# Kernel tuning notes

Measured on AMD Instinct MI355X. Metric: run time of the kernel, lower is better.

The kernel has to match this reference:

```python
import jax, jax.numpy as jnp
import numpy as np

N_NODES = 50000
N_EDGES = 600000
N_RELS = 19
D_IN = 128
D_HID = 64
D_OUT = 2


def setup_inputs() -> dict:
    key = jax.random.key(0)
    ks = jax.random.split(key, 10)
    feat = jax.random.normal(ks[0], (N_NODES, D_IN), dtype=jnp.float32)
    src = jax.random.randint(ks[1], (N_EDGES,), 0, N_NODES)
    dst = jax.random.randint(ks[2], (N_EDGES,), 0, N_NODES)
    etype = jax.random.randint(ks[3], (N_EDGES,), 0, N_RELS)
    s1 = 1.0 / np.sqrt(D_IN)
    s2 = 1.0 / np.sqrt(D_HID)
    W1 = jax.random.normal(ks[4], (N_RELS, D_IN, D_HID), dtype=jnp.float32) * s1
    loop1 = jax.random.normal(ks[5], (D_IN, D_HID), dtype=jnp.float32) * s1
    b1 = jnp.zeros((D_HID,), dtype=jnp.float32)
    W2 = jax.random.normal(ks[6], (N_RELS, D_HID, D_OUT), dtype=jnp.float32) * s2
    loop2 = jax.random.normal(ks[7], (D_HID, D_OUT), dtype=jnp.float32) * s2
    b2 = jnp.zeros((D_OUT,), dtype=jnp.float32)
    return {"feat": feat, "W1": W1, "loop1": loop1, "b1": b1,
            "W2": W2, "loop2": loop2, "b2": b2,
            "src": src, "dst": dst, "etype": etype}


def _rel_graph_conv(h, W, loop_w, bias, src, dst, etype, activation):
    # Per-relation transform of all nodes: [N, R, O]; then gather per edge.
    # (num_rels * out_feat is small, so this is cheaper than gathering W per edge.)
    transformed = jnp.einsum('nd,rdo->nro', h, W)
    msg = transformed[src, etype]                      # [E, O] edge messages
    agg = jax.ops.segment_sum(msg, dst, num_segments=h.shape[0])  # scatter-add
    out = agg + h @ loop_w + bias                      # self-loop + bias
    if activation is not None:
        out = activation(out)
    return out


def reference(feat, W1, loop1, b1, W2, loop2, b2, src, dst, etype):
    h = _rel_graph_conv(feat, W1, loop1, b1, src, dst, etype, jax.nn.relu)
    h = _rel_graph_conv(h, W2, loop2, b2, src, dst, etype, None)
    return h
```

## Files before the change

kernel.cpp:

```cpp
#include <hip/hip_runtime.h>

#define N_NODES 50000
#define N_EDGES 600000
#define N_RELS  19
#define D_IN    128
#define D_HID   64
#define D_OUT   2
#define EDGE_TILES ((N_EDGES + 127) / 128 + N_RELS)
#define SL_BLOCKS  ((N_NODES + 63) / 64)

typedef unsigned short u16;
typedef unsigned int   u32;
typedef __attribute__((ext_vector_type(8))) short sfrag;
typedef __attribute__((ext_vector_type(4))) float f32x4;

__device__ __forceinline__ u16 f2bf(float f){
  union { float f; u32 i; } v; v.f = f;
  u32 r = v.i + 0x7fffu + ((v.i >> 16) & 1u);
  return (u16)(r >> 16);
}
__device__ __forceinline__ float bf2f(u16 u){
  union { u32 i; float f; } v; v.i = ((u32)u) << 16; return v.f;
}

__global__ void k_prep(const float* __restrict__ W1, const float* __restrict__ loop1,
                       const float* __restrict__ W2,
                       u16* __restrict__ W1Tb, u16* __restrict__ loop1Tb,
                       u16* __restrict__ W2Tb, int* __restrict__ hist_rel,
                       int* __restrict__ hist_dst, int* __restrict__ gcnt){
  int idx = blockIdx.x * 256 + threadIdx.x;
  if (idx < N_RELS)  hist_rel[idx] = 0;
  if (idx < N_NODES) hist_dst[idx] = 0;
  if (idx == 0) gcnt[0] = 0;
  const int T1 = N_RELS * D_HID * D_IN;
  const int T2 = T1 + N_RELS * 16 * D_HID;
  const int T3 = T2 + D_HID * D_IN;
  if (idx < T1) {
    int r = idx / (D_HID * D_IN);
    int t = idx - r * (D_HID * D_IN);
    int j = t >> 7, d = t & 127;
    W1Tb[idx] = f2bf(W1[(r * D_IN + d) * D_HID + j]);
  } else if (idx < T2) {
    int k2 = idx - T1;
    int r = k2 / (16 * D_HID);
    int t = k2 - r * (16 * D_HID);
    int n = t >> 6, k = t & 63;
    W2Tb[k2] = (n < D_OUT) ? f2bf(W2[(r * D_HID + k) * D_OUT + n]) : (u16)0;
  } else if (idx < T3) {
    int k2 = idx - T2;
    int j = k2 >> 7, d = k2 & 127;
    loop1Tb[k2] = f2bf(loop1[d * D_HID + j]);
  }
}

__global__ __launch_bounds__(256) void k_fused_pre(const float* __restrict__ feat,
                                                   u16* __restrict__ featb,
                                                   const int* __restrict__ et,
                                                   const int* __restrict__ dst,
                                                   int* __restrict__ hist_rel,
                                                   int* __restrict__ hist_dst){
  int i = blockIdx.x * 256 + threadIdx.x;
  float2 f = ((const float2*)feat)[i];
  ((u32*)featb)[i] = (u32)f2bf(f.x) | ((u32)f2bf(f.y) << 16);
  if (blockIdx.x < (N_EDGES + 255) / 256) {
    __shared__ int lh[N_RELS];
    int tid = threadIdx.x;
    if (tid < N_RELS) lh[tid] = 0;
    __syncthreads();
    int e = blockIdx.x * 256 + tid;
    if (e < N_EDGES) {
      atomicAdd(&lh[et[e]], 1);
      atomicAdd(&hist_dst[dst[e]], 1);
    }
    __syncthreads();
    if (tid < N_RELS && lh[tid]) atomicAdd(&hist_rel[tid], lh[tid]);
  }
}

__global__ __launch_bounds__(256) void k_alloc_scan(
    const int* __restrict__ hist_dst, int* __restrict__ dstart,
    int* __restrict__ cur_dst, int* __restrict__ gcnt,
    const int* __restrict__ hist_rel, int* __restrict__ offs,
    int* __restrict__ toff, int* __restrict__ cur_rel){
  if (blockIdx.x == 196) {
    if (threadIdx.x == 0) {
      int acc = 0, tacc = 0;
      offs[0] = 0; toff[0] = 0;
      for (int r = 0; r < N_RELS; ++r) {
        cur_rel[r] = acc;
        int c = hist_rel[r];
        acc += c;                offs[r + 1] = acc;
        tacc += (c + 127) >> 7;  toff[r + 1] = tacc;
      }
    }
    return;
  }
  __shared__ int wbase[4];
  int tid = threadIdx.x, lane = tid & 63, wv = tid >> 6;
  int n = blockIdx.x * 256 + tid;
  int v = (n < N_NODES) ? hist_dst[n] : 0;
  int x = v;
  #pragma unroll
  for (int o = 1; o < 64; o <<= 1) { int u = __shfl_up(x, o); if (lane >= o) x += u; }
  if (lane == 63) wbase[wv] = atomicAdd(gcnt, x);
  __syncthreads();
  int start = wbase[wv] + x - v;
  if (n < N_NODES) { dstart[n] = start; cur_dst[n] = start; }
}

__global__ __launch_bounds__(256) void k_scatter_rel(const int* __restrict__ et,
                                                     int* __restrict__ cursor,
                                                     int* __restrict__ perm){
  __shared__ int lh[N_RELS], base[N_RELS];
  int tid = threadIdx.x;
  if (tid < N_RELS) lh[tid] = 0;
  __syncthreads();
  int e = blockIdx.x * 256 + tid;
  int r = 0, my = 0;
  bool valid = e < N_EDGES;
  if (valid) { r = et[e]; my = atomicAdd(&lh[r], 1); }
  __syncthreads();
  if (tid < N_RELS && lh[tid]) base[tid] = atomicAdd(&cursor[tid], lh[tid]);
  __syncthreads();
  if (valid) perm[base[r] + my] = e;
}

__global__ __launch_bounds__(256) void k_se1(
    const u16* __restrict__ featb, const u16* __restrict__ W1Tb,
    const u16* __restrict__ loop1Tb, const float* __restrict__ b1,
    const int* __restrict__ src, const int* __restrict__ dst,
    const int* __restrict__ perm, const int* __restrict__ offs,
    const int* __restrict__ toff, int* __restrict__ cur_dst,
    u16* __restrict__ msgbuf, float* __restrict__ agg1f){
  __shared__ __align__(16) u16 Als[128][136];
  __shared__ int posIds[128];
  int tid = threadIdx.x, lane = tid & 63, w = tid >> 6;
  int r16 = lane & 15, c4 = lane >> 4;

  if (blockIdx.x >= EDGE_TILES) {
    int base = (blockIdx.x - EDGE_TILES) * 64;
    { int i = tid >> 2, seg = tid & 3;
      int n = base + i; if (n >= N_NODES) n = N_NODES - 1;
      const uint4* g = (const uint4*)(featb + (size_t)n * D_IN) + seg * 4;
      uint4* d = (uint4*)&Als[i][seg * 32];
      d[0] = g[0]; d[1] = g[1]; d[2] = g[2]; d[3] = g[3]; }
    __syncthreads();
    sfrag aF[4];
    #pragma unroll
    for (int kk = 0; kk < 4; ++kk)
      aF[kk] = *(const sfrag*)&Als[w * 16 + r16][kk * 32 + c4 * 8];
    #pragma unroll
    for (int ct = 0; ct < 4; ++ct) {
      f32x4 acc = {0.f, 0.f, 0.f, 0.f};
      #pragma unroll
      for (int kk = 0; kk < 4; ++kk) {
        sfrag bF = *(const sfrag*)(loop1Tb + ((ct * 16 + r16) << 7) + kk * 32 + c4 * 8);
        acc = __builtin_amdgcn_mfma_f32_16x16x32_bf16(aF[kk], bF, acc, 0, 0, 0);
      }
      int col = ct * 16 + r16;
      float bias = b1[col];
      #pragma unroll
      for (int reg = 0; reg < 4; ++reg) {
        int row = base + w * 16 + c4 * 4 + reg;
        if (row < N_NODES) agg1f[(size_t)row * D_HID + col] = acc[reg] + bias;
      }
    }
    return;
  }

  int b = blockIdx.x;
  unsigned long long mm = __ballot((lane < N_RELS) && (b >= toff[lane + 1]));
  int rel = __popcll(mm);
  if (rel >= N_RELS) return;
  int ts = offs[rel] + ((b - toff[rel]) << 7);
  int vc = offs[rel + 1] - ts; if (vc > 128) vc = 128;

  #pragma unroll
  for (int p = 0; p < 2; ++p) {
    int i = p * 64 + (tid >> 2), seg = tid & 3;
    if (i < vc) {
      int e = perm[ts + i];
      if (seg == 0) posIds[i] = atomicAdd(&cur_dst[dst[e]], 1);
      const uint4* g = (const uint4*)(featb + (size_t)src[e] * D_IN) + seg * 4;
      uint4* d = (uint4*)&Als[i][seg * 32];
      d[0] = g[0]; d[1] = g[1]; d[2] = g[2]; d[3] = g[3];
    } else if (seg == 0) posIds[i] = -1;
  }
  __syncthreads();

  sfrag aF[2][4];
  #pragma unroll
  for (int mt = 0; mt < 2; ++mt)
    #pragma unroll
    for (int kk = 0; kk < 4; ++kk)
      aF[mt][kk] = *(const sfrag*)&Als[w * 32 + mt * 16 + r16][kk * 32 + c4 * 8];
  const u16* Wr = W1Tb + ((size_t)rel << 13);
  f32x4 accAll[2][4];
  #pragma unroll
  for (int ct = 0; ct < 4; ++ct) {
    #pragma unroll
    for (int mt = 0; mt < 2; ++mt) {
      f32x4 acc = {0.f, 0.f, 0.f, 0.f};
      #pragma unroll
      for (int kk = 0; kk < 4; ++kk) {
        sfrag bF = *(const sfrag*)(Wr + ((ct * 16 + r16) << 7) + kk * 32 + c4 * 8);
        acc = __builtin_amdgcn_mfma_f32_16x16x32_bf16(aF[mt][kk], bF, acc, 0, 0, 0);
      }
      accAll[mt][ct] = acc;
    }
  }
  float* msg = (float*)&Als[0][0];
  #pragma unroll
  for (int mt = 0; mt < 2; ++mt)
    #pragma unroll
    for (int ct = 0; ct < 4; ++ct) {
      int col = ct * 16 + r16;
      #pragma unroll
      for (int reg = 0; reg < 4; ++reg) {
        int row = w * 32 + mt * 16 + c4 * 4 + reg;
        msg[row * 68 + col] = accAll[mt][ct][reg];
      }
    }
  __syncthreads();
  { int row = tid >> 1, half = tid & 1;
    int pos = posIds[row];
    if (pos >= 0) {
      const float* mr = msg + row * 68 + half * 32;
      u32 pk[16];
      #pragma unroll
      for (int q = 0; q < 16; ++q)
        pk[q] = (u32)f2bf(mr[2 * q]) | ((u32)f2bf(mr[2 * q + 1]) << 16);
      uint4* d = (uint4*)(msgbuf + (size_t)pos * D_HID + half * 32);
      d[0] = *(uint4*)&pk[0];  d[1] = *(uint4*)&pk[4];
      d[2] = *(uint4*)&pk[8];  d[3] = *(uint4*)&pk[12];
    } }
}

__global__ __launch_bounds__(256) void k_agg_relu_self2(
    const u16* __restrict__ msgbuf, const int* __restrict__ dstart,
    const int* __restrict__ cnt, const float* __restrict__ agg1f,
    const float* __restrict__ loop2, const float* __restrict__ b2,
    u16* __restrict__ h1b, float* __restrict__ out){
  int wv = threadIdx.x >> 6, lane = threadIdx.x & 63;
  int n = blockIdx.x * 4 + wv;
  int s = dstart[n], epos = s + cnt[n];
  int h = lane >> 5, c = lane & 31;
  float a0 = 0.f, a1 = 0.f;
  for (int i = s + h; i < epos; i += 2) {
    u32 v = ((const u32*)msgbuf)[(size_t)i * 32 + c];
    a0 += bf2f((u16)(v & 0xffffu));
    a1 += bf2f((u16)(v >> 16));
  }
  a0 += __shfl_down(a0, 32);
  a1 += __shfl_down(a1, 32);
  float p0 = 0.f, p1 = 0.f;
  if (h == 0) {
    float2 sl = ((const float2*)(agg1f + (size_t)n * D_HID))[c];
    float v0 = a0 + sl.x, v1 = a1 + sl.y;
    v0 = v0 > 0.f ? v0 : 0.f;
    v1 = v1 > 0.f ? v1 : 0.f;
    ((u32*)h1b)[(size_t)n * 32 + c] = (u32)f2bf(v0) | ((u32)f2bf(v1) << 16);
    float2 w0 = ((const float2*)loop2)[2 * c];
    float2 w1 = ((const float2*)loop2)[2 * c + 1];
    p0 = v0 * w0.x + v1 * w1.x;
    p1 = v0 * w0.y + v1 * w1.y;
  }
  #pragma unroll
  for (int off = 16; off; off >>= 1) {
    p0 += __shfl_down(p0, off);
    p1 += __shfl_down(p1, off);
  }
  if (lane == 0) {
    out[n * 2]     = p0 + b2[0];
    out[n * 2 + 1] = p1 + b2[1];
  }
}

__global__ __launch_bounds__(256) void k_edge2_mfma(
    const u16* __restrict__ h1b, const u16* __restrict__ W2Tb,
    const int* __restrict__ src, const int* __restrict__ dst,
    const int* __restrict__ perm, const int* __restrict__ offs,
    const int* __restrict__ toff, float* __restrict__ out){
  __shared__ __align__(16) u16 Als[128][72];
  __shared__ __align__(16) u16 Bls[16][72];
  __shared__ int dstIds[128];
  int tid = threadIdx.x, lane = tid & 63, w = tid >> 6;

  int b = blockIdx.x;
  unsigned long long mm = __ballot((lane < N_RELS) && (b >= toff[lane + 1]));
  int rel = __popcll(mm);
  if (rel >= N_RELS) return;
  int ts = offs[rel] + ((b - toff[rel]) << 7);
  int vc = offs[rel + 1] - ts; if (vc > 128) vc = 128;

  if (tid < 128) {
    ((uint4*)&Bls[tid >> 3][0])[tid & 7] = ((const uint4*)(W2Tb + (size_t)rel * 16 * 64))[tid];
  }
  {
    int i = tid >> 1, half = tid & 1;
    if (i < vc) {
      int e = perm[ts + i];
      if (half == 0) dstIds[i] = dst[e];
      const uint4* g = (const uint4*)(h1b + (size_t)src[e] * D_HID) + half * 4;
      uint4* d = (uint4*)&Als[i][half * 32];
      d[0] = g[0]; d[1] = g[1]; d[2] = g[2]; d[3] = g[3];
    } else if (half == 0) dstIds[i] = -1;
  }
  __syncthreads();

  int r16 = lane & 15, c4 = lane >> 4;
  #pragma unroll
  for (int mt = 0; mt < 2; ++mt) {
    f32x4 acc = {0.f, 0.f, 0.f, 0.f};
    #pragma unroll
    for (int kk = 0; kk < 2; ++kk) {
      sfrag aF = *(const sfrag*)&Als[w * 32 + mt * 16 + r16][kk * 32 + c4 * 8];
      sfrag bF = *(const sfrag*)&Bls[r16][kk * 32 + c4 * 8];
      acc = __builtin_amdgcn_mfma_f32_16x16x32_bf16(aF, bF, acc, 0, 0, 0);
    }
    if (r16 < D_OUT) {
      #pragma unroll
      for (int reg = 0; reg < 4; ++reg) {
        int row = w * 32 + mt * 16 + c4 * 4 + reg;
        int dn = dstIds[row];
        if (dn >= 0) atomicAdd(&out[dn * D_OUT + r16], acc[reg]);
      }
    }
  }
}

extern "C" void kernel_launch(void* const* d_in, const int* in_sizes, int n_in,
                              void* d_out, int out_size, void* d_ws, size_t ws_size,
                              hipStream_t stream){
  const float* feat  = (const float*)d_in[0];
  const float* W1    = (const float*)d_in[1];
  const float* loop1 = (const float*)d_in[2];
  const float* b1    = (const float*)d_in[3];
  const float* W2    = (const float*)d_in[4];
  const float* loop2 = (const float*)d_in[5];
  const float* b2    = (const float*)d_in[6];
  const int* src     = (const int*)d_in[7];
  const int* dst     = (const int*)d_in[8];
  const int* et      = (const int*)d_in[9];
  float* out = (float*)d_out;

  char* w = (char*)d_ws;
  u16*   W1Tb     = (u16*)(w);
  u16*   W2Tb     = (u16*)(w + 311296);
  u16*   loop1Tb  = (u16*)(w + 350208);
  int*   hist_rel = (int*)(w + 366592);
  int*   offs     = (int*)(w + 366720);
  int*   toff     = (int*)(w + 366848);
  int*   cur_rel  = (int*)(w + 366976);
  int*   gcnt     = (int*)(w + 367104);
  int*   hist_dst = (int*)(w + 367232);
  int*   dstart   = (int*)(w + 567232);
  int*   cur_dst  = (int*)(w + 767232);
  int*   perm     = (int*)(w + 967232);
  u16*   featb    = (u16*)(w + 3367232);
  float* agg1f    = (float*)(w + 16167232);
  u16*   h1b      = (u16*)(w + 28967232);
  u16*   msgbuf   = (u16*)(w + 35367232);

  k_prep          <<<716,   256, 0, stream>>>(W1, loop1, W2, W1Tb, loop1Tb, W2Tb,
                                              hist_rel, hist_dst, gcnt);
  k_fused_pre     <<<12500, 256, 0, stream>>>(feat, featb, et, dst, hist_rel, hist_dst);
  k_alloc_scan    <<<197,   256, 0, stream>>>(hist_dst, dstart, cur_dst, gcnt,
                                              hist_rel, offs, toff, cur_rel);
  k_scatter_rel   <<<2344,  256, 0, stream>>>(et, cur_rel, perm);
  k_se1           <<<EDGE_TILES + SL_BLOCKS, 256, 0, stream>>>(
                      featb, W1Tb, loop1Tb, b1, src, dst, perm, offs, toff,
                      cur_dst, msgbuf, agg1f);
  k_agg_relu_self2<<<12500, 256, 0, stream>>>(msgbuf, dstart, hist_dst, agg1f,
                                              loop2, b2, h1b, out);
  k_edge2_mfma    <<<EDGE_TILES, 256, 0, stream>>>(h1b, W2Tb, src, dst, perm, offs, toff, out);
}
```

Baseline: 346.3 us.

## Precompute per-node layer-2 transform for all relations, gather scalars per edge

Layer 2 now computes, for each node, a 40-wide table: its hidden vector times every relation's W2 plus the self-loop, using one MFMA pass inside the aggregation kernel. A simple per-edge kernel then gathers two floats from that table and atomically adds them, replacing the per-relation tile kernel that gathered 64-wide bf16 rows per edge. Layer 1 also stages W1 and loop1 weight tiles in LDS instead of reading fragments straight from global memory. The cost is a 40-float-per-node table write and a per-node loop in the aggregation kernel with fewer blocks.

```diff
diff --git a/kernel.cpp b/kernel.cpp
--- a/kernel.cpp
+++ b/kernel.cpp
@@ -24,16 +24,16 @@
 }
 
 __global__ void k_prep(const float* __restrict__ W1, const float* __restrict__ loop1,
-                       const float* __restrict__ W2,
+                       const float* __restrict__ W2, const float* __restrict__ loop2,
                        u16* __restrict__ W1Tb, u16* __restrict__ loop1Tb,
-                       u16* __restrict__ W2Tb, int* __restrict__ hist_rel,
+                       u16* __restrict__ W2T2b, int* __restrict__ hist_rel,
                        int* __restrict__ hist_dst, int* __restrict__ gcnt){
   int idx = blockIdx.x * 256 + threadIdx.x;
   if (idx < N_RELS)  hist_rel[idx] = 0;
   if (idx < N_NODES) hist_dst[idx] = 0;
   if (idx == 0) gcnt[0] = 0;
   const int T1 = N_RELS * D_HID * D_IN;
-  const int T2 = T1 + N_RELS * 16 * D_HID;
+  const int T2 = T1 + 48 * D_HID;
   const int T3 = T2 + D_HID * D_IN;
   if (idx < T1) {
     int r = idx / (D_HID * D_IN);
@@ -42,10 +42,11 @@
     W1Tb[idx] = f2bf(W1[(r * D_IN + d) * D_HID + j]);
   } else if (idx < T2) {
     int k2 = idx - T1;
-    int r = k2 / (16 * D_HID);
-    int t = k2 - r * (16 * D_HID);
-    int n = t >> 6, k = t & 63;
-    W2Tb[k2] = (n < D_OUT) ? f2bf(W2[(r * D_HID + k) * D_OUT + n]) : (u16)0;
+    int j = k2 >> 6, d = k2 & 63;
+    float v = 0.f;
+    if (j < 2 * N_RELS)       v = W2[((j >> 1) * D_HID + d) * D_OUT + (j & 1)];
+    else if (j < 2 * N_RELS + 2) v = loop2[d * D_OUT + (j - 2 * N_RELS)];
+    W2T2b[k2] = f2bf(v);
   } else if (idx < T3) {
     int k2 = idx - T2;
     int j = k2 >> 7, d = k2 & 127;
@@ -133,12 +134,17 @@
     const int* __restrict__ toff, int* __restrict__ cur_dst,
     u16* __restrict__ msgbuf, float* __restrict__ agg1f){
   __shared__ __align__(16) u16 Als[128][136];
+  __shared__ __align__(16) u16 Bls[64][136];
   __shared__ int posIds[128];
   int tid = threadIdx.x, lane = tid & 63, w = tid >> 6;
   int r16 = lane & 15, c4 = lane >> 4;
 
   if (blockIdx.x >= EDGE_TILES) {
     int base = (blockIdx.x - EDGE_TILES) * 64;
+    { int j = tid >> 2, seg = tid & 3;
+      const uint4* g = (const uint4*)(loop1Tb + j * 128) + seg * 4;
+      uint4* d = (uint4*)&Bls[j][seg * 32];
+      d[0] = g[0]; d[1] = g[1]; d[2] = g[2]; d[3] = g[3]; }
     { int i = tid >> 2, seg = tid & 3;
       int n = base + i; if (n >= N_NODES) n = N_NODES - 1;
       const uint4* g = (const uint4*)(featb + (size_t)n * D_IN) + seg * 4;
@@ -154,7 +160,7 @@
       f32x4 acc = {0.f, 0.f, 0.f, 0.f};
       #pragma unroll
       for (int kk = 0; kk < 4; ++kk) {
-        sfrag bF = *(const sfrag*)(loop1Tb + ((ct * 16 + r16) << 7) + kk * 32 + c4 * 8);
+        sfrag bF = *(const sfrag*)&Bls[ct * 16 + r16][kk * 32 + c4 * 8];
         acc = __builtin_amdgcn_mfma_f32_16x16x32_bf16(aF[kk], bF, acc, 0, 0, 0);
       }
       int col = ct * 16 + r16;
@@ -175,6 +181,12 @@
   int ts = offs[rel] + ((b - toff[rel]) << 7);
   int vc = offs[rel + 1] - ts; if (vc > 128) vc = 128;
 
+  {
+    int j = tid >> 2, seg = tid & 3;
+    const uint4* g = (const uint4*)(W1Tb + ((size_t)rel * 64 + j) * 128) + seg * 4;
+    uint4* d = (uint4*)&Bls[j][seg * 32];
+    d[0] = g[0]; d[1] = g[1]; d[2] = g[2]; d[3] = g[3];
+  }
   #pragma unroll
   for (int p = 0; p < 2; ++p) {
     int i = p * 64 + (tid >> 2), seg = tid & 3;
@@ -194,18 +206,19 @@
     #pragma unroll
     for (int kk = 0; kk < 4; ++kk)
       aF[mt][kk] = *(const sfrag*)&Als[w * 32 + mt * 16 + r16][kk * 32 + c4 * 8];
-  const u16* Wr = W1Tb + ((size_t)rel << 13);
   f32x4 accAll[2][4];
   #pragma unroll
   for (int ct = 0; ct < 4; ++ct) {
+    sfrag bF[4];
+    #pragma unroll
+    for (int kk = 0; kk < 4; ++kk)
+      bF[kk] = *(const sfrag*)&Bls[ct * 16 + r16][kk * 32 + c4 * 8];
     #pragma unroll
     for (int mt = 0; mt < 2; ++mt) {
       f32x4 acc = {0.f, 0.f, 0.f, 0.f};
       #pragma unroll
-      for (int kk = 0; kk < 4; ++kk) {
-        sfrag bF = *(const sfrag*)(Wr + ((ct * 16 + r16) << 7) + kk * 32 + c4 * 8);
-        acc = __builtin_amdgcn_mfma_f32_16x16x32_bf16(aF[mt][kk], bF, acc, 0, 0, 0);
-      }
+      for (int kk = 0; kk < 4; ++kk)
+        acc = __builtin_amdgcn_mfma_f32_16x16x32_bf16(aF[mt][kk], bF[kk], acc, 0, 0, 0);
       accAll[mt][ct] = acc;
     }
   }
@@ -236,96 +249,84 @@
     } }
 }
 
-__global__ __launch_bounds__(256) void k_agg_relu_self2(
+__global__ __launch_bounds__(256) void k_agg_t(
     const u16* __restrict__ msgbuf, const int* __restrict__ dstart,
     const int* __restrict__ cnt, const float* __restrict__ agg1f,
-    const float* __restrict__ loop2, const float* __restrict__ b2,
-    u16* __restrict__ h1b, float* __restrict__ out){
-  int wv = threadIdx.x >> 6, lane = threadIdx.x & 63;
-  int n = blockIdx.x * 4 + wv;
-  int s = dstart[n], epos = s + cnt[n];
+    const u16* __restrict__ W2T2b, const float* __restrict__ b2,
+    float* __restrict__ Tmat, float* __restrict__ out){
+  __shared__ __align__(16) u16 Hls[64][72];
+  __shared__ __align__(16) u16 Bls[48][72];
+  int tid = threadIdx.x, lane = tid & 63, w = tid >> 6;
+  int n0 = blockIdx.x * 64;
+  #pragma unroll
+  for (int p = 0; p < 2; ++p) {
+    int idx = p * 256 + tid;
+    if (idx < 384) ((uint4*)&Bls[idx >> 3][0])[idx & 7] = ((const uint4*)W2T2b)[idx];
+  }
   int h = lane >> 5, c = lane & 31;
-  float a0 = 0.f, a1 = 0.f;
-  for (int i = s + h; i < epos; i += 2) {
-    u32 v = ((const u32*)msgbuf)[(size_t)i * 32 + c];
-    a0 += bf2f((u16)(v & 0xffffu));
-    a1 += bf2f((u16)(v >> 16));
-  }
-  a0 += __shfl_down(a0, 32);
-  a1 += __shfl_down(a1, 32);
-  float p0 = 0.f, p1 = 0.f;
-  if (h == 0) {
-    float2 sl = ((const float2*)(agg1f + (size_t)n * D_HID))[c];
-    float v0 = a0 + sl.x, v1 = a1 + sl.y;
-    v0 = v0 > 0.f ? v0 : 0.f;
-    v1 = v1 > 0.f ? v1 : 0.f;
-    ((u32*)h1b)[(size_t)n * 32 + c] = (u32)f2bf(v0) | ((u32)f2bf(v1) << 16);
-    float2 w0 = ((const float2*)loop2)[2 * c];
-    float2 w1 = ((const float2*)loop2)[2 * c + 1];
-    p0 = v0 * w0.x + v1 * w1.x;
-    p1 = v0 * w0.y + v1 * w1.y;
-  }
-  #pragma unroll
-  for (int off = 16; off; off >>= 1) {
-    p0 += __shfl_down(p0, off);
-    p1 += __shfl_down(p1, off);
-  }
-  if (lane == 0) {
-    out[n * 2]     = p0 + b2[0];
-    out[n * 2 + 1] = p1 + b2[1];
-  }
-}
-
-__global__ __launch_bounds__(256) void k_edge2_mfma(
-    const u16* __restrict__ h1b, const u16* __restrict__ W2Tb,
-    const int* __restrict__ src, const int* __restrict__ dst,
-    const int* __restrict__ perm, const int* __restrict__ offs,
-    const int* __restrict__ toff, float* __restrict__ out){
-  __shared__ __align__(16) u16 Als[128][72];
-  __shared__ __align__(16) u16 Bls[16][72];
-  __shared__ int dstIds[128];
-  int tid = threadIdx.x, lane = tid & 63, w = tid >> 6;
-
-  int b = blockIdx.x;
-  unsigned long long mm = __ballot((lane < N_RELS) && (b >= toff[lane + 1]));
-  int rel = __popcll(mm);
-  if (rel >= N_RELS) return;
-  int ts = offs[rel] + ((b - toff[rel]) << 7);
-  int vc = offs[rel + 1] - ts; if (vc > 128) vc = 128;
-
-  if (tid < 128) {
-    ((uint4*)&Bls[tid >> 3][0])[tid & 7] = ((const uint4*)(W2Tb + (size_t)rel * 16 * 64))[tid];
-  }
-  {
-    int i = tid >> 1, half = tid & 1;
-    if (i < vc) {
-      int e = perm[ts + i];
-      if (half == 0) dstIds[i] = dst[e];
-      const uint4* g = (const uint4*)(h1b + (size_t)src[e] * D_HID) + half * 4;
-      uint4* d = (uint4*)&Als[i][half * 32];
-      d[0] = g[0]; d[1] = g[1]; d[2] = g[2]; d[3] = g[3];
-    } else if (half == 0) dstIds[i] = -1;
-  }
-  __syncthreads();
-
+  for (int t = 0; t < 16; ++t) {
+    int i = w * 16 + t, n = n0 + i;
+    float a0 = 0.f, a1 = 0.f;
+    if (n < N_NODES) {
+      int s = dstart[n], epos = s + cnt[n];
+      for (int q = s + h; q < epos; q += 2) {
+        u32 v = ((const u32*)msgbuf)[(size_t)q * 32 + c];
+        a0 += bf2f((u16)(v & 0xffffu));
+        a1 += bf2f((u16)(v >> 16));
+      }
+    }
+    a0 += __shfl_down(a0, 32);
+    a1 += __shfl_down(a1, 32);
+    if (h == 0) {
+      u32 pk = 0;
+      if (n < N_NODES) {
+        float2 sl = ((const float2*)(agg1f + (size_t)n * D_HID))[c];
+        float v0 = a0 + sl.x, v1 = a1 + sl.y;
+        v0 = v0 > 0.f ? v0 : 0.f;
+        v1 = v1 > 0.f ? v1 : 0.f;
+        pk = (u32)f2bf(v0) | ((u32)f2bf(v1) << 16);
+      }
+      *(u32*)&Hls[i][2 * c] = pk;
+    }
+  }
+  __syncthreads();
   int r16 = lane & 15, c4 = lane >> 4;
-  #pragma unroll
-  for (int mt = 0; mt < 2; ++mt) {
+  sfrag aF[2];
+  aF[0] = *(const sfrag*)&Hls[w * 16 + r16][c4 * 8];
+  aF[1] = *(const sfrag*)&Hls[w * 16 + r16][32 + c4 * 8];
+  #pragma unroll
+  for (int ct = 0; ct < 3; ++ct) {
     f32x4 acc = {0.f, 0.f, 0.f, 0.f};
     #pragma unroll
     for (int kk = 0; kk < 2; ++kk) {
-      sfrag aF = *(const sfrag*)&Als[w * 32 + mt * 16 + r16][kk * 32 + c4 * 8];
-      sfrag bF = *(const sfrag*)&Bls[r16][kk * 32 + c4 * 8];
-      acc = __builtin_amdgcn_mfma_f32_16x16x32_bf16(aF, bF, acc, 0, 0, 0);
-    }
-    if (r16 < D_OUT) {
-      #pragma unroll
-      for (int reg = 0; reg < 4; ++reg) {
-        int row = w * 32 + mt * 16 + c4 * 4 + reg;
-        int dn = dstIds[row];
-        if (dn >= 0) atomicAdd(&out[dn * D_OUT + r16], acc[reg]);
-      }
-    }
+      sfrag bF = *(const sfrag*)&Bls[ct * 16 + r16][kk * 32 + c4 * 8];
+      acc = __builtin_amdgcn_mfma_f32_16x16x32_bf16(aF[kk], bF, acc, 0, 0, 0);
+    }
+    int col = ct * 16 + r16;
+    #pragma unroll
+    for (int reg = 0; reg < 4; ++reg) {
+      int row = w * 16 + c4 * 4 + reg;
+      int n = n0 + row;
+      if (n < N_NODES && col < 40) {
+        float v = acc[reg];
+        Tmat[(size_t)n * 40 + col] = v;
+        if (col >= 38) out[n * 2 + (col - 38)] = v + b2[col - 38];
+      }
+    }
+  }
+}
+
+__global__ __launch_bounds__(256) void k_edge2s(const int* __restrict__ src,
+                                                const int* __restrict__ dst,
+                                                const int* __restrict__ et,
+                                                const float* __restrict__ Tmat,
+                                                float* __restrict__ out){
+  int e = blockIdx.x * 256 + threadIdx.x;
+  if (e < N_EDGES) {
+    int s = src[e], d = dst[e], r = et[e];
+    float2 tv = *(const float2*)(Tmat + (size_t)s * 40 + 2 * r);
+    atomicAdd(&out[d * 2],     tv.x);
+    atomicAdd(&out[d * 2 + 1], tv.y);
   }
 }
 
@@ -346,32 +347,32 @@
 
   char* w = (char*)d_ws;
   u16*   W1Tb     = (u16*)(w);
-  u16*   W2Tb     = (u16*)(w + 311296);
-  u16*   loop1Tb  = (u16*)(w + 350208);
-  int*   hist_rel = (int*)(w + 366592);
-  int*   offs     = (int*)(w + 366720);
-  int*   toff     = (int*)(w + 366848);
-  int*   cur_rel  = (int*)(w + 366976);
-  int*   gcnt     = (int*)(w + 367104);
-  int*   hist_dst = (int*)(w + 367232);
-  int*   dstart   = (int*)(w + 567232);
-  int*   cur_dst  = (int*)(w + 767232);
-  int*   perm     = (int*)(w + 967232);
-  u16*   featb    = (u16*)(w + 3367232);
-  float* agg1f    = (float*)(w + 16167232);
-  u16*   h1b      = (u16*)(w + 28967232);
-  u16*   msgbuf   = (u16*)(w + 35367232);
-
-  k_prep          <<<716,   256, 0, stream>>>(W1, loop1, W2, W1Tb, loop1Tb, W2Tb,
-                                              hist_rel, hist_dst, gcnt);
-  k_fused_pre     <<<12500, 256, 0, stream>>>(feat, featb, et, dst, hist_rel, hist_dst);
-  k_alloc_scan    <<<197,   256, 0, stream>>>(hist_dst, dstart, cur_dst, gcnt,
-                                              hist_rel, offs, toff, cur_rel);
-  k_scatter_rel   <<<2344,  256, 0, stream>>>(et, cur_rel, perm);
-  k_se1           <<<EDGE_TILES + SL_BLOCKS, 256, 0, stream>>>(
-                      featb, W1Tb, loop1Tb, b1, src, dst, perm, offs, toff,
-                      cur_dst, msgbuf, agg1f);
-  k_agg_relu_self2<<<12500, 256, 0, stream>>>(msgbuf, dstart, hist_dst, agg1f,
-                                              loop2, b2, h1b, out);
-  k_edge2_mfma    <<<EDGE_TILES, 256, 0, stream>>>(h1b, W2Tb, src, dst, perm, offs, toff, out);
-}
+  u16*   W2T2b    = (u16*)(w + 311296);
+  u16*   loop1Tb  = (u16*)(w + 317440);
+  int*   hist_rel = (int*)(w + 333824);
+  int*   offs     = (int*)(w + 333952);
+  int*   toff     = (int*)(w + 334080);
+  int*   cur_rel  = (int*)(w + 334208);
+  int*   gcnt     = (int*)(w + 334336);
+  int*   hist_dst = (int*)(w + 334464);
+  int*   dstart   = (int*)(w + 534464);
+  int*   cur_dst  = (int*)(w + 734464);
+  int*   perm     = (int*)(w + 934464);
+  u16*   featb    = (u16*)(w + 3334464);
+  float* agg1f    = (float*)(w + 16134464);
+  float* Tmat     = (float*)(w + 28934464);
+  u16*   msgbuf   = (u16*)(w + 36934464);
+
+  k_prep       <<<652,   256, 0, stream>>>(W1, loop1, W2, loop2, W1Tb, loop1Tb, W2T2b,
+                                           hist_rel, hist_dst, gcnt);
+  k_fused_pre  <<<12500, 256, 0, stream>>>(feat, featb, et, dst, hist_rel, hist_dst);
+  k_alloc_scan <<<197,   256, 0, stream>>>(hist_dst, dstart, cur_dst, gcnt,
+                                           hist_rel, offs, toff, cur_rel);
+  k_scatter_rel<<<2344,  256, 0, stream>>>(et, cur_rel, perm);
+  k_se1        <<<EDGE_TILES + SL_BLOCKS, 256, 0, stream>>>(
+                   featb, W1Tb, loop1Tb, b1, src, dst, perm, offs, toff,
+                   cur_dst, msgbuf, agg1f);
+  k_agg_t      <<<SL_BLOCKS, 256, 0, stream>>>(msgbuf, dstart, hist_dst, agg1f,
+                                               W2T2b, b2, Tmat, out);
+  k_edge2s     <<<2344,  256, 0, stream>>>(src, dst, et, Tmat, out);
+}
```

Result: slower. 373.1 us (+7.7%).
